# Optimization experiments

Measured on AMD Instinct MI355X. Metric: run time of the kernel, lower is better.

Reference implementation:

```python
import jax, jax.numpy as jnp
import numpy as np

N = 50000      # nodes
E = 800000     # edges
D_IN = 128     # embedding_dim
H = 4          # g_num_heads
D = 64         # g_hidden_dim (per head)
SLOPE = 0.2    # g_negative_slope


def setup_inputs() -> dict:
    key = jax.random.key(0)
    ks = jax.random.split(key, 16)
    def lin(k, fin, fout):
        return jax.random.normal(k, (fin, fout), jnp.float32) / np.float32(np.sqrt(fin))
    def att(k, heads):
        return jax.random.normal(k, (heads, D), jnp.float32) * np.float32(0.1)
    return {
        'x':  jax.random.normal(ks[0], (N, D_IN), jnp.float32),
        'src': jax.random.randint(ks[1], (E,), 0, N),
        'dst': jax.random.randint(ks[2], (E,), 0, N),
        'W0': lin(ks[3], D_IN, H * D), 'al0': att(ks[4], H), 'ar0': att(ks[5], H), 'b0': jnp.zeros((H * D,), jnp.float32),
        'W1': lin(ks[6], H * D, H * D), 'al1': att(ks[7], H), 'ar1': att(ks[8], H), 'b1': jnp.zeros((H * D,), jnp.float32),
        'W2': lin(ks[9], H * D, 1 * D), 'al2': att(ks[10], 1), 'ar2': att(ks[11], 1), 'b2': jnp.zeros((D,), jnp.float32),
    }


def gat_layer(x, W, al, ar, b, src, dst, heads, act):
    # x: [N, F_in] -> h: [N, heads, D]
    h = (x @ W).reshape(N, heads, D)
    el = jnp.sum(h * al, axis=-1)                      # [N, heads]
    er = jnp.sum(h * ar, axis=-1)                      # [N, heads]
    e = jax.nn.leaky_relu(el[src] + er[dst], SLOPE)    # [E, heads]
    # edge softmax over incoming edges of each dst node (numerically stable)
    m = jax.ops.segment_max(e, dst, num_segments=N)    # [N, heads]
    ee = jnp.exp(e - m[dst])
    z = jax.ops.segment_sum(ee, dst, num_segments=N)   # [N, heads]
    alpha = ee / z[dst]                                # [E, heads]
    # weighted aggregation of source features
    out = jax.ops.segment_sum(alpha[:, :, None] * h[src], dst, num_segments=N)  # [N, heads, D]
    out = out + b.reshape(1, heads, D)
    return jax.nn.elu(out) if act else out


def reference(x, src, dst, W0, al0, ar0, b0, W1, al1, ar1, b1, W2, al2, ar2, b2):
    f = gat_layer(x, W0, al0, ar0, b0, src, dst, H, True).reshape(N, H * D)
    f = gat_layer(f, W1, al1, ar1, b1, src, dst, H, True).reshape(N, H * D)
    out = gat_layer(f, W2, al2, ar2, b2, src, dst, 1, False).mean(axis=1)  # [N, D]
    return out
```

## Files before the change

kernel.cpp:

```cpp
#include <hip/hip_runtime.h>
#include <math.h>

#define NNODES 50000
#define NEDGES 800000


__global__ void k_zero_int(int* __restrict__ p, int n) {
  int i = blockIdx.x * blockDim.x + threadIdx.x;
  if (i < n) p[i] = 0;
}

__global__ void k_hist(const int* __restrict__ dst, int* __restrict__ deg) {
  int i = blockIdx.x * blockDim.x + threadIdx.x;
  if (i < NEDGES) atomicAdd(&deg[dst[i]], 1);
}

__global__ __launch_bounds__(1024) void k_scan(const int* __restrict__ deg,
                                               int* __restrict__ ptr,
                                               int* __restrict__ cur) {
  __shared__ int s_w[16];
  __shared__ int s_carry;
  const int tid = threadIdx.x;
  const int lane = tid & 63;
  const int wid = tid >> 6;
  if (tid == 0) s_carry = 0;
  __syncthreads();
  for (int base = 0; base < NNODES; base += 1024) {
    const int i = base + tid;
    const int v = (i < NNODES) ? deg[i] : 0;
    int x = v;
#pragma unroll
    for (int off = 1; off < 64; off <<= 1) {
      int t = __shfl_up(x, off);
      if (lane >= off) x += t;
    }
    if (lane == 63) s_w[wid] = x;
    __syncthreads();
    const int carry = s_carry;
    if (wid == 0) {
      int ws = (lane < 16) ? s_w[lane] : 0;
#pragma unroll
      for (int off = 1; off < 16; off <<= 1) {
        int t = __shfl_up(ws, off);
        if (lane >= off) ws += t;
      }
      if (lane < 16) s_w[lane] = ws;
    }
    __syncthreads();
    const int woff = (wid > 0) ? s_w[wid - 1] : 0;
    const int excl = carry + woff + (x - v);
    if (i < NNODES) {
      ptr[i] = excl;
      cur[i] = excl;
    }
    __syncthreads();
    if (tid == 0) s_carry = carry + s_w[15];
  }
  __syncthreads();
  if (tid == 0) ptr[NNODES] = s_carry;
}

__global__ void k_scatter(const int* __restrict__ src, const int* __restrict__ dst,
                          int* __restrict__ cur, int* __restrict__ csr) {
  int i = blockIdx.x * blockDim.x + threadIdx.x;
  if (i < NEDGES) {
    int d = dst[i];
    int p = atomicAdd(&cur[d], 1);
    csr[p] = src[i];
  }
}


template <int K, int NC, int BN, int HEADS>
__global__ __launch_bounds__(256) void k_gemm(const float* __restrict__ A,
                                              const float* __restrict__ B,
                                              float* __restrict__ C,
                                              const float* __restrict__ al,
                                              const float* __restrict__ ar,
                                              float* __restrict__ el,
                                              float* __restrict__ er) {
  constexpr int BM = 128;
  constexpr int BK = 16;
  constexpr int TN = BN / 16;
  __shared__ float Ast[BK][BM + 4];
  __shared__ float Bs[BK][BN];
  const int tid = threadIdx.x;
  const int tx = tid & 15;
  const int ty = tid >> 4;
  const int rowBase = blockIdx.x * BM;
  const int colBase = blockIdx.y * BN;
  const int arow = tid >> 2;
  const int ak = (tid & 3) << 2;
  const bool v0 = (rowBase + arow) < NNODES;
  const bool v1 = (rowBase + arow + 64) < NNODES;
  const float* a0p = A + (size_t)(rowBase + arow) * K + ak;
  const float* a1p = A + (size_t)(rowBase + arow + 64) * K + ak;

  float4 avr[2];
  float4 bvr[2];
  const float4 z4 = make_float4(0.f, 0.f, 0.f, 0.f);

  auto load_tile = [&](int k0) {
    avr[0] = v0 ? *(const float4*)(a0p + k0) : z4;
    avr[1] = v1 ? *(const float4*)(a1p + k0) : z4;
    if constexpr (BN == 128) {
      const int brow = tid >> 5;
      const int bcol = (tid & 31) << 2;
      bvr[0] = *(const float4*)&B[(size_t)(k0 + brow) * NC + colBase + bcol];
      bvr[1] = *(const float4*)&B[(size_t)(k0 + brow + 8) * NC + colBase + bcol];
    } else {
      const int brow = tid >> 4;
      const int bcol = (tid & 15) << 2;
      bvr[0] = *(const float4*)&B[(size_t)(k0 + brow) * NC + colBase + bcol];
    }
  };

  float acc[8][TN] = {};
  load_tile(0);

  for (int k0 = 0; k0 < K; k0 += BK) {
#pragma unroll
    for (int rr = 0; rr < 2; ++rr) {
      const int r = arow + rr * 64;
      Ast[ak + 0][r] = avr[rr].x;
      Ast[ak + 1][r] = avr[rr].y;
      Ast[ak + 2][r] = avr[rr].z;
      Ast[ak + 3][r] = avr[rr].w;
    }
    if constexpr (BN == 128) {
      const int brow = tid >> 5;
      const int bcol = (tid & 31) << 2;
      *(float4*)&Bs[brow][bcol] = bvr[0];
      *(float4*)&Bs[brow + 8][bcol] = bvr[1];
    } else {
      const int brow = tid >> 4;
      const int bcol = (tid & 15) << 2;
      *(float4*)&Bs[brow][bcol] = bvr[0];
    }
    __syncthreads();
    if (k0 + BK < K) load_tile(k0 + BK);
#pragma unroll
    for (int k = 0; k < BK; ++k) {
      float4 fa0 = *(const float4*)&Ast[k][ty * 8];
      float4 fa1 = *(const float4*)&Ast[k][ty * 8 + 4];
      float a[8] = {fa0.x, fa0.y, fa0.z, fa0.w, fa1.x, fa1.y, fa1.z, fa1.w};
      float b[TN];
      float4 b0 = *(const float4*)&Bs[k][tx * 4];
      b[0] = b0.x; b[1] = b0.y; b[2] = b0.z; b[3] = b0.w;
      if constexpr (TN == 8) {
        float4 b1 = *(const float4*)&Bs[k][64 + tx * 4];
        b[4] = b1.x; b[5] = b1.y; b[6] = b1.z; b[7] = b1.w;
      }
#pragma unroll
      for (int i = 0; i < 8; ++i)
#pragma unroll
        for (int j = 0; j < TN; ++j) acc[i][j] = fmaf(a[i], b[j], acc[i][j]);
    }
    __syncthreads();
  }

  const int head0 = colBase >> 6;
  float4 alA = *(const float4*)&al[colBase + tx * 4];
  float4 arA = *(const float4*)&ar[colBase + tx * 4];
  float4 alB = z4, arB = z4;
  if constexpr (TN == 8) {
    alB = *(const float4*)&al[colBase + 64 + tx * 4];
    arB = *(const float4*)&ar[colBase + 64 + tx * 4];
  }

#pragma unroll
  for (int i = 0; i < 8; ++i) {
    const int r = rowBase + ty * 8 + i;
    const bool vr = r < NNODES;
    if (vr) {
      float4 o = make_float4(acc[i][0], acc[i][1], acc[i][2], acc[i][3]);
      *(float4*)&C[(size_t)r * NC + colBase + tx * 4] = o;
      if constexpr (TN == 8) {
        float4 o2 = make_float4(acc[i][4], acc[i][5], acc[i][6], acc[i][7]);
        *(float4*)&C[(size_t)r * NC + colBase + 64 + tx * 4] = o2;
      }
    }
    float pea = acc[i][0] * alA.x + acc[i][1] * alA.y + acc[i][2] * alA.z + acc[i][3] * alA.w;
    float pra = acc[i][0] * arA.x + acc[i][1] * arA.y + acc[i][2] * arA.z + acc[i][3] * arA.w;
    float peb = 0.f, prb = 0.f;
    if constexpr (TN == 8) {
      peb = acc[i][4] * alB.x + acc[i][5] * alB.y + acc[i][6] * alB.z + acc[i][7] * alB.w;
      prb = acc[i][4] * arB.x + acc[i][5] * arB.y + acc[i][6] * arB.z + acc[i][7] * arB.w;
    }
#pragma unroll
    for (int m = 1; m < 16; m <<= 1) {
      pea += __shfl_xor(pea, m);
      pra += __shfl_xor(pra, m);
      if constexpr (TN == 8) {
        peb += __shfl_xor(peb, m);
        prb += __shfl_xor(prb, m);
      }
    }
    if (tx == 0 && vr) {
      el[r * HEADS + head0] = pea;
      er[r * HEADS + head0] = pra;
      if constexpr (TN == 8) {
        el[r * HEADS + head0 + 1] = peb;
        er[r * HEADS + head0 + 1] = prb;
      }
    }
  }
}


template <int HEADS, bool ACT>
__global__ __launch_bounds__(64) void k_aggregate(const float* __restrict__ h,
                                                  const float* __restrict__ el,
                                                  const float* __restrict__ er,
                                                  const int* __restrict__ ptr,
                                                  const int* __restrict__ csr,
                                                  const float* __restrict__ bias,
                                                  float* __restrict__ out) {
  constexpr int HD = HEADS * 64;
  constexpr int VEC = HEADS;
  constexpr int CH = 64 / HEADS;
  const int n = blockIdx.x;
  const int tid = threadIdx.x;
  const int head = tid / (64 / HEADS);
  const int beg = ptr[n];
  const int deg = ptr[n + 1] - beg;

  __shared__ float s_z[HEADS];
  __shared__ int s_src[CH];
  __shared__ float s_w[64];

  const int hh = tid & (HEADS - 1);
  const int cslot = tid / HEADS;
  const float ern = er[n * HEADS + hh];

  float zacc = 0.f;
  float acc[VEC];
#pragma unroll
  for (int v = 0; v < VEC; ++v) acc[v] = 0.f;

  for (int c0 = 0; c0 < deg; c0 += CH) {
    const int cnt = min(CH, deg - c0);
    __syncthreads();
    if (cslot < cnt) {
      int s = csr[beg + c0 + cslot];
      if (hh == 0) s_src[cslot] = s;
      float e = el[s * HEADS + hh] + ern;
      e = e > 0.f ? e : 0.2f * e;
      float w = expf(e);
      s_w[tid] = w;
      zacc += w;
    }
    __syncthreads();
    for (int c = 0; c < cnt; ++c) {
      const float w = s_w[c * HEADS + head];
      const float* hp = &h[(size_t)s_src[c] * HD + tid * VEC];
      if constexpr (VEC == 4) {
        float4 hv = *(const float4*)hp;
        acc[0] = fmaf(w, hv.x, acc[0]);
        acc[1] = fmaf(w, hv.y, acc[1]);
        acc[2] = fmaf(w, hv.z, acc[2]);
        acc[3] = fmaf(w, hv.w, acc[3]);
      } else {
        acc[0] = fmaf(w, hp[0], acc[0]);
      }
    }
  }

#pragma unroll
  for (int m = HEADS; m < 64; m <<= 1) zacc += __shfl_xor(zacc, m);
  if (tid < HEADS) s_z[tid] = zacc;
  __syncthreads();
  const float invz = (deg > 0) ? 1.0f / s_z[head] : 0.f;

#pragma unroll
  for (int v = 0; v < VEC; ++v) {
    float r = acc[v] * invz + bias[tid * VEC + v];
    if (ACT) r = r > 0.f ? r : expm1f(r);
    acc[v] = r;
  }
  if constexpr (VEC == 4) {
    float4 o = make_float4(acc[0], acc[1], acc[2], acc[3]);
    *(float4*)&out[(size_t)n * HD + (tid << 2)] = o;
  } else {
    out[(size_t)n * HD + tid] = acc[0];
  }
}


extern "C" void kernel_launch(void* const* d_in, const int* in_sizes, int n_in,
                              void* d_out, int out_size, void* d_ws, size_t ws_size,
                              hipStream_t stream) {
  const float* x   = (const float*)d_in[0];
  const int*   src = (const int*)d_in[1];
  const int*   dst = (const int*)d_in[2];
  const float* W0  = (const float*)d_in[3];
  const float* al0 = (const float*)d_in[4];
  const float* ar0 = (const float*)d_in[5];
  const float* b0  = (const float*)d_in[6];
  const float* W1  = (const float*)d_in[7];
  const float* al1 = (const float*)d_in[8];
  const float* ar1 = (const float*)d_in[9];
  const float* b1  = (const float*)d_in[10];
  const float* W2  = (const float*)d_in[11];
  const float* al2 = (const float*)d_in[12];
  const float* ar2 = (const float*)d_in[13];
  const float* b2  = (const float*)d_in[14];
  float* out = (float*)d_out;

  float* hA = (float*)d_ws;
  float* fB = hA + (size_t)NNODES * 256;
  float* el = fB + (size_t)NNODES * 256;
  float* er = el + (size_t)NNODES * 4;
  int* deg  = (int*)(er + (size_t)NNODES * 4);
  int* ptr  = deg + NNODES;
  int* cur  = ptr + NNODES + 1;
  int* csr  = cur + NNODES;

  k_zero_int<<<(NNODES + 255) / 256, 256, 0, stream>>>(deg, NNODES);
  k_hist<<<(NEDGES + 255) / 256, 256, 0, stream>>>(dst, deg);
  k_scan<<<1, 1024, 0, stream>>>(deg, ptr, cur);
  k_scatter<<<(NEDGES + 255) / 256, 256, 0, stream>>>(src, dst, cur, csr);

  dim3 g128((NNODES + 127) / 128, 256 / 128);
  k_gemm<128, 256, 128, 4><<<g128, 256, 0, stream>>>(x, W0, hA, al0, ar0, el, er);
  k_aggregate<4, true><<<NNODES, 64, 0, stream>>>(hA, el, er, ptr, csr, b0, fB);
  k_gemm<256, 256, 128, 4><<<g128, 256, 0, stream>>>(fB, W1, hA, al1, ar1, el, er);
  k_aggregate<4, true><<<NNODES, 64, 0, stream>>>(hA, el, er, ptr, csr, b1, fB);
  dim3 g2((NNODES + 127) / 128, 1);
  k_gemm<256, 64, 64, 1><<<g2, 256, 0, stream>>>(fB, W2, hA, al2, ar2, el, er);
  k_aggregate<1, false><<<NNODES, 64, 0, stream>>>(hA, el, er, ptr, csr, b2, out);
}
```

Before: 729.8 us.

## Double-buffer GEMM tiles with direct global-to-LDS loads and smaller row tiles

Restructures the node-feature GEMM to use double-buffered LDS tiles. B is loaded straight into shared memory with global_load_lds, and the next A tile is prefetched while the current one is computed. The row tile shrinks from 128 to 64 with an occupancy hint of 4 blocks per CU, which doubles the block count and lowers per-thread register use. The aim is to hide global load latency and improve occupancy, at the cost of less reuse per block and reliance on correct async-load synchronization.

```diff
diff --git a/kernel.cpp b/kernel.cpp
--- a/kernel.cpp
+++ b/kernel.cpp
@@ -3,6 +3,11 @@
 
 #define NNODES 50000
 #define NEDGES 800000
+
+__device__ __forceinline__ void gll16(const float* g, float* l) {
+  __builtin_amdgcn_global_load_lds((const __attribute__((address_space(1))) void*)g,
+                                   (__attribute__((address_space(3))) void*)l, 16, 0, 0);
+}
 
 
 __global__ void k_zero_int(int* __restrict__ p, int n) {
@@ -72,112 +77,109 @@
 
 
 template <int K, int NC, int BN, int HEADS>
-__global__ __launch_bounds__(256) void k_gemm(const float* __restrict__ A,
-                                              const float* __restrict__ B,
-                                              float* __restrict__ C,
-                                              const float* __restrict__ al,
-                                              const float* __restrict__ ar,
-                                              float* __restrict__ el,
-                                              float* __restrict__ er) {
-  constexpr int BM = 128;
+__global__ __launch_bounds__(256, 4) void k_gemm(const float* __restrict__ A,
+                                                 const float* __restrict__ B,
+                                                 float* __restrict__ C,
+                                                 const float* __restrict__ al,
+                                                 const float* __restrict__ ar,
+                                                 float* __restrict__ el,
+                                                 float* __restrict__ er) {
+  constexpr int BM = 64;
   constexpr int BK = 16;
   constexpr int TN = BN / 16;
-  __shared__ float Ast[BK][BM + 4];
-  __shared__ float Bs[BK][BN];
+  constexpr int T = K / BK;
+  __shared__ float Ast[2][BK][BM + 4];
+  __shared__ float Bs[2][BK][BN];
   const int tid = threadIdx.x;
   const int tx = tid & 15;
   const int ty = tid >> 4;
+  const int wv = tid >> 6;
+  const int l = tid & 63;
   const int rowBase = blockIdx.x * BM;
   const int colBase = blockIdx.y * BN;
   const int arow = tid >> 2;
   const int ak = (tid & 3) << 2;
-  const bool v0 = (rowBase + arow) < NNODES;
-  const bool v1 = (rowBase + arow + 64) < NNODES;
-  const float* a0p = A + (size_t)(rowBase + arow) * K + ak;
-  const float* a1p = A + (size_t)(rowBase + arow + 64) * K + ak;
-
-  float4 avr[2];
-  float4 bvr[2];
+  const bool va = (rowBase + arow) < NNODES;
+  const float* ap = A + (size_t)(rowBase + arow) * K + ak;
   const float4 z4 = make_float4(0.f, 0.f, 0.f, 0.f);
 
-  auto load_tile = [&](int k0) {
-    avr[0] = v0 ? *(const float4*)(a0p + k0) : z4;
-    avr[1] = v1 ? *(const float4*)(a1p + k0) : z4;
+  auto stage_B = [&](int k0, int buf) {
     if constexpr (BN == 128) {
-      const int brow = tid >> 5;
-      const int bcol = (tid & 31) << 2;
-      bvr[0] = *(const float4*)&B[(size_t)(k0 + brow) * NC + colBase + bcol];
-      bvr[1] = *(const float4*)&B[(size_t)(k0 + brow + 8) * NC + colBase + bcol];
+#pragma unroll
+      for (int j = 0; j < 2; ++j) {
+        const int row = 4 * wv + 2 * j + (l >> 5);
+        gll16(&B[(size_t)(k0 + row) * NC + colBase + ((l & 31) << 2)],
+              &Bs[buf][4 * wv + 2 * j][0]);
+      }
     } else {
-      const int brow = tid >> 4;
-      const int bcol = (tid & 15) << 2;
-      bvr[0] = *(const float4*)&B[(size_t)(k0 + brow) * NC + colBase + bcol];
+      const int row = 4 * wv + (l >> 4);
+      gll16(&B[(size_t)(k0 + row) * NC + colBase + ((l & 15) << 2)],
+            &Bs[buf][4 * wv][0]);
     }
   };
 
-  float acc[8][TN] = {};
-  load_tile(0);
-
-  for (int k0 = 0; k0 < K; k0 += BK) {
-#pragma unroll
-    for (int rr = 0; rr < 2; ++rr) {
-      const int r = arow + rr * 64;
-      Ast[ak + 0][r] = avr[rr].x;
-      Ast[ak + 1][r] = avr[rr].y;
-      Ast[ak + 2][r] = avr[rr].z;
-      Ast[ak + 3][r] = avr[rr].w;
-    }
-    if constexpr (BN == 128) {
-      const int brow = tid >> 5;
-      const int bcol = (tid & 31) << 2;
-      *(float4*)&Bs[brow][bcol] = bvr[0];
-      *(float4*)&Bs[brow + 8][bcol] = bvr[1];
-    } else {
-      const int brow = tid >> 4;
-      const int bcol = (tid & 15) << 2;
-      *(float4*)&Bs[brow][bcol] = bvr[0];
-    }
-    __syncthreads();
-    if (k0 + BK < K) load_tile(k0 + BK);
+  float4 avr;
+  float acc[4][TN] = {};
+
+  stage_B(0, 0);
+  avr = va ? *(const float4*)ap : z4;
+  Ast[0][ak + 0][arow] = avr.x;
+  Ast[0][ak + 1][arow] = avr.y;
+  Ast[0][ak + 2][arow] = avr.z;
+  Ast[0][ak + 3][arow] = avr.w;
+  __syncthreads();
+
+  for (int t = 0; t < T; ++t) {
+    const int cur = t & 1;
+    const int nxt = cur ^ 1;
+    if (t + 1 < T) {
+      stage_B((t + 1) * BK, nxt);
+      avr = va ? *(const float4*)(ap + (t + 1) * BK) : z4;
+    }
 #pragma unroll
     for (int k = 0; k < BK; ++k) {
-      float4 fa0 = *(const float4*)&Ast[k][ty * 8];
-      float4 fa1 = *(const float4*)&Ast[k][ty * 8 + 4];
-      float a[8] = {fa0.x, fa0.y, fa0.z, fa0.w, fa1.x, fa1.y, fa1.z, fa1.w};
+      float4 fa = *(const float4*)&Ast[cur][k][ty << 2];
+      float a[4] = {fa.x, fa.y, fa.z, fa.w};
       float b[TN];
-      float4 b0 = *(const float4*)&Bs[k][tx * 4];
+      float4 b0 = *(const float4*)&Bs[cur][k][tx << 2];
       b[0] = b0.x; b[1] = b0.y; b[2] = b0.z; b[3] = b0.w;
       if constexpr (TN == 8) {
-        float4 b1 = *(const float4*)&Bs[k][64 + tx * 4];
+        float4 b1 = *(const float4*)&Bs[cur][k][64 + (tx << 2)];
         b[4] = b1.x; b[5] = b1.y; b[6] = b1.z; b[7] = b1.w;
       }
 #pragma unroll
-      for (int i = 0; i < 8; ++i)
+      for (int i = 0; i < 4; ++i)
 #pragma unroll
         for (int j = 0; j < TN; ++j) acc[i][j] = fmaf(a[i], b[j], acc[i][j]);
     }
+    if (t + 1 < T) {
+      Ast[nxt][ak + 0][arow] = avr.x;
+      Ast[nxt][ak + 1][arow] = avr.y;
+      Ast[nxt][ak + 2][arow] = avr.z;
+      Ast[nxt][ak + 3][arow] = avr.w;
+    }
     __syncthreads();
   }
 
   const int head0 = colBase >> 6;
-  float4 alA = *(const float4*)&al[colBase + tx * 4];
-  float4 arA = *(const float4*)&ar[colBase + tx * 4];
+  float4 alA = *(const float4*)&al[colBase + (tx << 2)];
+  float4 arA = *(const float4*)&ar[colBase + (tx << 2)];
   float4 alB = z4, arB = z4;
   if constexpr (TN == 8) {
-    alB = *(const float4*)&al[colBase + 64 + tx * 4];
-    arB = *(const float4*)&ar[colBase + 64 + tx * 4];
-  }
-
-#pragma unroll
-  for (int i = 0; i < 8; ++i) {
-    const int r = rowBase + ty * 8 + i;
+    alB = *(const float4*)&al[colBase + 64 + (tx << 2)];
+    arB = *(const float4*)&ar[colBase + 64 + (tx << 2)];
+  }
+
+#pragma unroll
+  for (int i = 0; i < 4; ++i) {
+    const int r = rowBase + (ty << 2) + i;
     const bool vr = r < NNODES;
     if (vr) {
       float4 o = make_float4(acc[i][0], acc[i][1], acc[i][2], acc[i][3]);
-      *(float4*)&C[(size_t)r * NC + colBase + tx * 4] = o;
+      *(float4*)&C[(size_t)r * NC + colBase + (tx << 2)] = o;
       if constexpr (TN == 8) {
         float4 o2 = make_float4(acc[i][4], acc[i][5], acc[i][6], acc[i][7]);
-        *(float4*)&C[(size_t)r * NC + colBase + 64 + tx * 4] = o2;
+        *(float4*)&C[(size_t)r * NC + colBase + 64 + (tx << 2)] = o2;
       }
     }
     float pea = acc[i][0] * alA.x + acc[i][1] * alA.y + acc[i][2] * alA.z + acc[i][3] * alA.w;
@@ -321,12 +323,12 @@
   k_scan<<<1, 1024, 0, stream>>>(deg, ptr, cur);
   k_scatter<<<(NEDGES + 255) / 256, 256, 0, stream>>>(src, dst, cur, csr);
 
-  dim3 g128((NNODES + 127) / 128, 256 / 128);
-  k_gemm<128, 256, 128, 4><<<g128, 256, 0, stream>>>(x, W0, hA, al0, ar0, el, er);
+  dim3 g01((NNODES + 63) / 64, 256 / 128);
+  k_gemm<128, 256, 128, 4><<<g01, 256, 0, stream>>>(x, W0, hA, al0, ar0, el, er);
   k_aggregate<4, true><<<NNODES, 64, 0, stream>>>(hA, el, er, ptr, csr, b0, fB);
-  k_gemm<256, 256, 128, 4><<<g128, 256, 0, stream>>>(fB, W1, hA, al1, ar1, el, er);
+  k_gemm<256, 256, 128, 4><<<g01, 256, 0, stream>>>(fB, W1, hA, al1, ar1, el, er);
   k_aggregate<4, true><<<NNODES, 64, 0, stream>>>(hA, el, er, ptr, csr, b1, fB);
-  dim3 g2((NNODES + 127) / 128, 1);
+  dim3 g2((NNODES + 63) / 64, 1);
   k_gemm<256, 64, 64, 1><<<g2, 256, 0, stream>>>(fB, W2, hA, al2, ar2, el, er);
   k_aggregate<1, false><<<NNODES, 64, 0, stream>>>(hA, el, er, ptr, csr, b2, out);
 }
```

New measurement: 1.046 ms. 1.43x slower.
